# Optimization experiments

Measured on AMD Instinct MI355X. Metric: run time of the kernel, lower is better.

## Reference

```python
import jax, jax.numpy as jnp
import numpy as np
from functools import partial

B, T, I, H = 64, 1024, 256, 256


def _lstm_dir(x_tbi, w_ih, w_hh, b_ih, b_hh, reverse):
    """Coupled-gate LSTM over time. x_tbi: [T,B,I]. Returns hs [T,B,H], (hT, cT).

    Gates = x@W_ih^T + b_ih + h@W_hh^T + b_hh, split into (in, cell, out);
    forget = 1 - in (coupled input/forget gates).
    """
    Bn = x_tbi.shape[1]
    Hn = w_hh.shape[1]
    # Precompute input contribution for all timesteps in one big GEMM.
    gx = jnp.einsum('tbi,gi->tbg', x_tbi, w_ih) + (b_ih + b_hh)  # [T,B,3H]

    def step(carry, g):
        h, c = carry
        gates = g + h @ w_hh.T  # [B,3H]
        ig, cg, og = jnp.split(gates, 3, axis=1)
        ig = jax.nn.sigmoid(ig)
        fg = 1.0 - ig
        cg = jnp.tanh(cg)
        og = jax.nn.sigmoid(og)
        c = fg * c + ig * cg
        h = og * jnp.tanh(c)
        return (h, c), h

    h0 = jnp.zeros((Bn, Hn), dtype=x_tbi.dtype)
    c0 = jnp.zeros((Bn, Hn), dtype=x_tbi.dtype)
    # lax.scan(reverse=True) runs backward in time but stacks outputs in
    # original time order, matching ReverseLSTMLayer's reverse(outputs).
    (hT, cT), hs = jax.lax.scan(step, (h0, c0), gx, reverse=reverse)
    return hs, hT, cT


def setup_inputs() -> dict:
    key = jax.random.key(0)
    ks = jax.random.split(key, 9)
    s = 0.05  # small init scale for numerical sanity
    return {
        'X': jax.random.normal(ks[0], (B, T, I), dtype=jnp.float32),
        'wih_f': jax.random.normal(ks[1], (3 * H, I), dtype=jnp.float32) * s,
        'whh_f': jax.random.normal(ks[2], (3 * H, H), dtype=jnp.float32) * s,
        'bih_f': jax.random.normal(ks[3], (3 * H,), dtype=jnp.float32) * s,
        'bhh_f': jax.random.normal(ks[4], (3 * H,), dtype=jnp.float32) * s,
        'wih_b': jax.random.normal(ks[5], (3 * H, I), dtype=jnp.float32) * s,
        'whh_b': jax.random.normal(ks[6], (3 * H, H), dtype=jnp.float32) * s,
        'bih_b': jax.random.normal(ks[7], (3 * H,), dtype=jnp.float32) * s,
        'bhh_b': jax.random.normal(ks[8], (3 * H,), dtype=jnp.float32) * s,
    }


def reference(X, wih_f, whh_f, bih_f, bhh_f, wih_b, whh_b, bih_b, bhh_b):
    x_tbi = jnp.transpose(X, (1, 0, 2))  # [T,B,I]
    hs_f, hTf, cTf = _lstm_dir(x_tbi, wih_f, whh_f, bih_f, bhh_f, reverse=False)
    hs_b, hTb, cTb = _lstm_dir(x_tbi, wih_b, whh_b, bih_b, bhh_b, reverse=True)
    out = jnp.concatenate([hs_f, hs_b], axis=-1)  # [T,B,2H]
    hn = jnp.concatenate([hTf, hTb], axis=1)[None]  # [1,B,2H]
    cn = jnp.concatenate([cTf, cTb], axis=1)[None]
    return out, hn, cn
```

## Files before the change

### kernel.cpp

```cpp
#include <hip/hip_runtime.h>
#include <cstdint>
#include <cstddef>

#define TT 1024
#define NB 64
#define HD 256
#define NG 768

typedef short bhalf8 __attribute__((ext_vector_type(8)));
typedef float f32x4  __attribute__((ext_vector_type(4)));

__device__ __forceinline__ unsigned short f2bf(float f) {
  unsigned u = __float_as_uint(f);
  unsigned r = (u + 0x7FFFu + ((u >> 16) & 1u)) >> 16;
  return (unsigned short)r;
}
__device__ __forceinline__ float bf2f(unsigned short s) {
  return __uint_as_float(((unsigned)s) << 16);
}
__device__ __forceinline__ float sigm(float x) {
  return __builtin_amdgcn_rcpf(1.0f + __expf(-x));
}
__device__ __forceinline__ float tanh_fast(float x) {
  return 1.0f - 2.0f * __builtin_amdgcn_rcpf(__expf(2.0f * x) + 1.0f);
}

#define GX_SLICE ((size_t)TT * NG * 16)

__launch_bounds__(256, 2)
__global__ void gx_kernel(const float* __restrict__ X,
                          const float* __restrict__ wih_f, const float* __restrict__ bih_f,
                          const float* __restrict__ bhh_f,
                          const float* __restrict__ wih_b, const float* __restrict__ bih_b,
                          const float* __restrict__ bhh_b,
                          unsigned short* __restrict__ gx) {
  const int tid = threadIdx.x;
  const int n0  = blockIdx.x * 64;
  const int t0  = blockIdx.y * 4;

  __shared__ unsigned short Al[64][264];
  __shared__ unsigned short Bl[64][264];

  const int lane = tid & 63, w = tid >> 6, quad = lane >> 4, l15 = lane & 15;

  for (int dir = 0; dir < 2; ++dir) {
    const float* wih = dir ? wih_b : wih_f;
    const float* bih = dir ? bih_b : bih_f;
    const float* bhh = dir ? bhh_b : bhh_f;
    unsigned short* gxd = gx + (size_t)dir * 4 * GX_SLICE;

    __syncthreads();
#pragma unroll
    for (int i = 0; i < 16; ++i) {
      int f4  = tid + i * 256;
      int row = f4 >> 6;
      int kk  = (f4 & 63) * 4;
      float4 wv = *(const float4*)(wih + (size_t)(n0 + row) * HD + kk);
      Bl[row][kk + 0] = f2bf(wv.x); Bl[row][kk + 1] = f2bf(wv.y);
      Bl[row][kk + 2] = f2bf(wv.z); Bl[row][kk + 3] = f2bf(wv.w);
    }

    for (int tt = 0; tt < 4; ++tt) {
      const int t = t0 + tt;
      __syncthreads();
#pragma unroll
      for (int i = 0; i < 16; ++i) {
        int f4  = tid + i * 256;
        int row = f4 >> 6;
        int kk  = (f4 & 63) * 4;
        float4 xv = *(const float4*)(X + ((size_t)row * TT + t) * HD + kk);
        Al[row][kk + 0] = f2bf(xv.x); Al[row][kk + 1] = f2bf(xv.y);
        Al[row][kk + 2] = f2bf(xv.z); Al[row][kk + 3] = f2bf(xv.w);
      }
      __syncthreads();

      f32x4 acc[4];
#pragma unroll
      for (int jt = 0; jt < 4; ++jt) { acc[jt][0]=0.f; acc[jt][1]=0.f; acc[jt][2]=0.f; acc[jt][3]=0.f; }

#pragma unroll
      for (int kt = 0; kt < 8; ++kt) {
        bhalf8 a = *(const bhalf8*)&Al[16 * w + l15][kt * 32 + quad * 8];
#pragma unroll
        for (int jt = 0; jt < 4; ++jt) {
          bhalf8 b = *(const bhalf8*)&Bl[jt * 16 + l15][kt * 32 + quad * 8];
          acc[jt] = __builtin_amdgcn_mfma_f32_16x16x32_bf16(a, b, acc[jt], 0, 0, 0);
        }
      }

      unsigned short* gs = gxd + w * GX_SLICE + (size_t)t * NG * 16;
#pragma unroll
      for (int jt = 0; jt < 4; ++jt) {
        int g = n0 + jt * 16 + l15;
        float bias = bih[g] + bhh[g];
        ushort4 pk;
        pk.x = f2bf(acc[jt][0] + bias); pk.y = f2bf(acc[jt][1] + bias);
        pk.z = f2bf(acc[jt][2] + bias); pk.w = f2bf(acc[jt][3] + bias);
        *(ushort4*)(gs + g * 16 + quad * 4) = pk;
      }
    }
  }
}

__attribute__((amdgpu_flat_work_group_size(512, 512)))
__attribute__((amdgpu_waves_per_eu(2, 2)))
__global__ void rec_kernel(const float* __restrict__ whh_f,
                           const float* __restrict__ whh_b,
                           const unsigned short* __restrict__ gx,
                           float* __restrict__ out) {
  const int tid  = threadIdx.x;
  const int lane = tid & 63, w = tid >> 6, quad = lane >> 4, l15 = lane & 15;
  const int blk = blockIdx.x;
  const int dir = blk >> 2;
  const int b0  = (blk & 3) * 16;
  const float* whh = dir ? whh_b : whh_f;
  const unsigned short* gxd = gx + (size_t)dir * 4 * GX_SLICE + (size_t)(blk & 3) * GX_SLICE;
  float* hn = out + (size_t)TT * NB * 512;
  float* cn = hn + (size_t)NB * 512;

  __shared__ uint4 wlds[8][8][64];
  __shared__ uint4 hk[2][8][64];

  bhalf8 wreg[5][8];
#pragma unroll
  for (int p = 0; p < 6; ++p) {
    int n = (p >> 1) * 256 + 32 * w + (p & 1) * 16 + l15;
#pragma unroll
    for (int kt = 0; kt < 8; ++kt) {
      const float* wp = whh + (size_t)n * HD + kt * 32 + quad * 8;
      float4 v0 = *(const float4*)wp;
      float4 v1 = *(const float4*)(wp + 4);
      union { unsigned short us[8]; bhalf8 v; uint4 u; } pk;
      pk.us[0] = f2bf(v0.x); pk.us[1] = f2bf(v0.y); pk.us[2] = f2bf(v0.z); pk.us[3] = f2bf(v0.w);
      pk.us[4] = f2bf(v1.x); pk.us[5] = f2bf(v1.y); pk.us[6] = f2bf(v1.z); pk.us[7] = f2bf(v1.w);
      if (p < 5) wreg[p][kt] = pk.v;
      else       wlds[w][kt][lane] = pk.u;
    }
  }

  {
    uint4 z; z.x = z.y = z.z = z.w = 0;
    for (int i = tid; i < 8 * 64; i += 512) ((uint4*)hk[0])[i] = z;
  }

  float cstate[2][4];
#pragma unroll
  for (int jn = 0; jn < 2; ++jn)
#pragma unroll
    for (int r = 0; r < 4; ++r) cstate[jn][r] = 0.0f;

  int goff[6];
#pragma unroll
  for (int p = 0; p < 6; ++p) {
    int g = (p >> 1) * 256 + 32 * w + (p & 1) * 16 + l15;
    goff[p] = g * 16 + quad * 4;
  }

  __syncthreads();

  const unsigned short* gptr = gxd + (size_t)(dir ? (TT - 1) : 0) * NG * 16;
  const ptrdiff_t gstep = dir ? -(ptrdiff_t)((size_t)NG * 16) : (ptrdiff_t)((size_t)NG * 16);

  ushort4 gxv[6];
#pragma unroll
  for (int p = 0; p < 6; ++p) gxv[p] = *(const ushort4*)(gptr + goff[p]);

#pragma unroll 2
  for (int s = 0; s < TT; ++s) {
    const int tr = dir ? (TT - 1 - s) : s;
    const int pb = s & 1;

    f32x4 acc[6];
#pragma unroll
    for (int p = 0; p < 6; ++p) {
      acc[p][0] = bf2f(gxv[p].x); acc[p][1] = bf2f(gxv[p].y);
      acc[p][2] = bf2f(gxv[p].z); acc[p][3] = bf2f(gxv[p].w);
    }
    gptr += gstep;
#pragma unroll
    for (int p = 0; p < 6; ++p) gxv[p] = *(const ushort4*)(gptr + goff[p]);

#pragma unroll
    for (int kt = 0; kt < 8; ++kt) {
      bhalf8 a = __builtin_bit_cast(bhalf8, hk[pb][kt][lane]);
#pragma unroll
      for (int p = 0; p < 5; ++p)
        acc[p] = __builtin_amdgcn_mfma_f32_16x16x32_bf16(a, wreg[p][kt], acc[p], 0, 0, 0);
      acc[5] = __builtin_amdgcn_mfma_f32_16x16x32_bf16(
          a, __builtin_bit_cast(bhalf8, wlds[w][kt][lane]), acc[5], 0, 0, 0);
    }

    float* orow = out + ((size_t)tr * NB + b0 + quad * 4) * 512 + dir * 256 + 32 * w + l15;
    unsigned short* hnext = (unsigned short*)hk[pb ^ 1][w];
#pragma unroll
    for (int jn = 0; jn < 2; ++jn) {
#pragma unroll
      for (int r = 0; r < 4; ++r) {
        float ig = sigm(acc[jn][r]);
        float cg = tanh_fast(acc[2 + jn][r]);
        float og = sigm(acc[4 + jn][r]);
        float cp = cstate[jn][r];
        float cv = __builtin_fmaf(ig, cg - cp, cp);
        cstate[jn][r] = cv;
        float hv = og * tanh_fast(cv);
        orow[(size_t)r * 512 + jn * 16] = hv;
        int chunk = (jn * 2 + (l15 >> 3)) * 16 + quad * 4 + r;
        hnext[chunk * 8 + (l15 & 7)] = f2bf(hv);
        if (s == TT - 1) {
          int brow = b0 + quad * 4 + r;
          int col  = 32 * w + jn * 16 + l15;
          hn[(size_t)brow * 512 + dir * 256 + col] = hv;
          cn[(size_t)brow * 512 + dir * 256 + col] = cv;
        }
      }
    }
    __syncthreads();
  }
}

extern "C" void kernel_launch(void* const* d_in, const int* in_sizes, int n_in,
                              void* d_out, int out_size, void* d_ws, size_t ws_size,
                              hipStream_t stream) {
  const float* X     = (const float*)d_in[0];
  const float* wih_f = (const float*)d_in[1];
  const float* whh_f = (const float*)d_in[2];
  const float* bih_f = (const float*)d_in[3];
  const float* bhh_f = (const float*)d_in[4];
  const float* wih_b = (const float*)d_in[5];
  const float* whh_b = (const float*)d_in[6];
  const float* bih_b = (const float*)d_in[7];
  const float* bhh_b = (const float*)d_in[8];
  float* out = (float*)d_out;
  unsigned short* gxbuf = (unsigned short*)d_ws;

  dim3 g1(NG / 64, TT / 4);
  gx_kernel<<<g1, 256, 0, stream>>>(X, wih_f, bih_f, bhh_f, wih_b, bih_b, bhh_b, gxbuf);
  rec_kernel<<<8, 512, 0, stream>>>(whh_f, whh_b, gxbuf, out);
}
```

Before: 2.264 ms.

## Prescale gates by log2e, batch reciprocals, use packed bf16 conversions

Folds the log2(e) (and 2*log2(e) for the cell gate) scaling into the input and recurrent weights and biases, so the recurrent step can call exp2 directly on pre-scaled gate values. It replaces the per-element reciprocals with a batched four-way reciprocal trick (one rcp per four values) and uses the hardware packed bf16 conversion instead of manual rounding. It also replaces the per-step output-row address computation with an incremented pointer. These changes shorten the serial per-timestep elementwise critical path, at the cost of extra rounding from the product-of-four reciprocal and clamping exponent inputs to ±24.

```diff
diff --git a/kernel.cpp b/kernel.cpp
--- a/kernel.cpp
+++ b/kernel.cpp
@@ -10,19 +10,32 @@
 typedef short bhalf8 __attribute__((ext_vector_type(8)));
 typedef float f32x4  __attribute__((ext_vector_type(4)));
 
-__device__ __forceinline__ unsigned short f2bf(float f) {
-  unsigned u = __float_as_uint(f);
-  unsigned r = (u + 0x7FFFu + ((u >> 16) & 1u)) >> 16;
-  return (unsigned short)r;
-}
+#define LOG2E  1.4426950408889634f
+#define LOG2E2 2.8853900817779268f
+
 __device__ __forceinline__ float bf2f(unsigned short s) {
   return __uint_as_float(((unsigned)s) << 16);
 }
-__device__ __forceinline__ float sigm(float x) {
-  return __builtin_amdgcn_rcpf(1.0f + __expf(-x));
-}
-__device__ __forceinline__ float tanh_fast(float x) {
-  return 1.0f - 2.0f * __builtin_amdgcn_rcpf(__expf(2.0f * x) + 1.0f);
+__device__ __forceinline__ unsigned cvt_pk_bf16(float lo, float hi) {
+  unsigned r;
+  asm("v_cvt_pk_bf16_f32 %0, %1, %2" : "=v"(r) : "v"(lo), "v"(hi));
+  return r;
+}
+__device__ __forceinline__ float clamp24(float x) {
+  return fminf(fmaxf(x, -24.0f), 24.0f);
+}
+__device__ __forceinline__ void inv4(float d0, float d1, float d2, float d3,
+                                     float& i0, float& i1, float& i2, float& i3) {
+  float p2 = d0 * d1;
+  float p3 = p2 * d2;
+  float p4 = p3 * d3;
+  float r  = __builtin_amdgcn_rcpf(p4);
+  i3 = r * p3;
+  float r3 = r * d3;
+  i2 = r3 * p2;
+  float r2 = r3 * d2;
+  i1 = r2 * d0;
+  i0 = r2 * d1;
 }
 
 #define GX_SLICE ((size_t)TT * NG * 16)
@@ -42,6 +55,7 @@
   __shared__ unsigned short Bl[64][264];
 
   const int lane = tid & 63, w = tid >> 6, quad = lane >> 4, l15 = lane & 15;
+  const float wsc = (n0 >= 256 && n0 < 512) ? LOG2E2 : LOG2E;
 
   for (int dir = 0; dir < 2; ++dir) {
     const float* wih = dir ? wih_b : wih_f;
@@ -56,8 +70,10 @@
       int row = f4 >> 6;
       int kk  = (f4 & 63) * 4;
       float4 wv = *(const float4*)(wih + (size_t)(n0 + row) * HD + kk);
-      Bl[row][kk + 0] = f2bf(wv.x); Bl[row][kk + 1] = f2bf(wv.y);
-      Bl[row][kk + 2] = f2bf(wv.z); Bl[row][kk + 3] = f2bf(wv.w);
+      uint2 p;
+      p.x = cvt_pk_bf16(wv.x * wsc, wv.y * wsc);
+      p.y = cvt_pk_bf16(wv.z * wsc, wv.w * wsc);
+      *(uint2*)&Bl[row][kk] = p;
     }
 
     for (int tt = 0; tt < 4; ++tt) {
@@ -69,8 +85,10 @@
         int row = f4 >> 6;
         int kk  = (f4 & 63) * 4;
         float4 xv = *(const float4*)(X + ((size_t)row * TT + t) * HD + kk);
-        Al[row][kk + 0] = f2bf(xv.x); Al[row][kk + 1] = f2bf(xv.y);
-        Al[row][kk + 2] = f2bf(xv.z); Al[row][kk + 3] = f2bf(xv.w);
+        uint2 p;
+        p.x = cvt_pk_bf16(xv.x, xv.y);
+        p.y = cvt_pk_bf16(xv.z, xv.w);
+        *(uint2*)&Al[row][kk] = p;
       }
       __syncthreads();
 
@@ -92,11 +110,11 @@
 #pragma unroll
       for (int jt = 0; jt < 4; ++jt) {
         int g = n0 + jt * 16 + l15;
-        float bias = bih[g] + bhh[g];
-        ushort4 pk;
-        pk.x = f2bf(acc[jt][0] + bias); pk.y = f2bf(acc[jt][1] + bias);
-        pk.z = f2bf(acc[jt][2] + bias); pk.w = f2bf(acc[jt][3] + bias);
-        *(ushort4*)(gs + g * 16 + quad * 4) = pk;
+        float bias = (bih[g] + bhh[g]) * wsc;
+        uint2 p;
+        p.x = cvt_pk_bf16(acc[jt][0] + bias, acc[jt][1] + bias);
+        p.y = cvt_pk_bf16(acc[jt][2] + bias, acc[jt][3] + bias);
+        *(uint2*)(gs + g * 16 + quad * 4) = p;
       }
     }
   }
@@ -125,14 +143,17 @@
 #pragma unroll
   for (int p = 0; p < 6; ++p) {
     int n = (p >> 1) * 256 + 32 * w + (p & 1) * 16 + l15;
+    const float wscp = ((p >> 1) == 1) ? LOG2E2 : LOG2E;
 #pragma unroll
     for (int kt = 0; kt < 8; ++kt) {
       const float* wp = whh + (size_t)n * HD + kt * 32 + quad * 8;
       float4 v0 = *(const float4*)wp;
       float4 v1 = *(const float4*)(wp + 4);
-      union { unsigned short us[8]; bhalf8 v; uint4 u; } pk;
-      pk.us[0] = f2bf(v0.x); pk.us[1] = f2bf(v0.y); pk.us[2] = f2bf(v0.z); pk.us[3] = f2bf(v0.w);
-      pk.us[4] = f2bf(v1.x); pk.us[5] = f2bf(v1.y); pk.us[6] = f2bf(v1.z); pk.us[7] = f2bf(v1.w);
+      union { bhalf8 v; uint4 u; } pk;
+      pk.u.x = cvt_pk_bf16(v0.x * wscp, v0.y * wscp);
+      pk.u.y = cvt_pk_bf16(v0.z * wscp, v0.w * wscp);
+      pk.u.z = cvt_pk_bf16(v1.x * wscp, v1.y * wscp);
+      pk.u.w = cvt_pk_bf16(v1.z * wscp, v1.w * wscp);
       if (p < 5) wreg[p][kt] = pk.v;
       else       wlds[w][kt][lane] = pk.u;
     }
@@ -161,13 +182,16 @@
   const unsigned short* gptr = gxd + (size_t)(dir ? (TT - 1) : 0) * NG * 16;
   const ptrdiff_t gstep = dir ? -(ptrdiff_t)((size_t)NG * 16) : (ptrdiff_t)((size_t)NG * 16);
 
+  float* orow = out + ((size_t)(dir ? (TT - 1) : 0) * NB + b0 + quad * 4) * 512
+                + dir * 256 + 32 * w + l15;
+  const ptrdiff_t ostep = dir ? -(ptrdiff_t)(NB * 512) : (ptrdiff_t)(NB * 512);
+
   ushort4 gxv[6];
 #pragma unroll
   for (int p = 0; p < 6; ++p) gxv[p] = *(const ushort4*)(gptr + goff[p]);
 
 #pragma unroll 2
   for (int s = 0; s < TT; ++s) {
-    const int tr = dir ? (TT - 1 - s) : s;
     const int pb = s & 1;
 
     f32x4 acc[6];
@@ -190,30 +214,62 @@
           a, __builtin_bit_cast(bhalf8, wlds[w][kt][lane]), acc[5], 0, 0, 0);
     }
 
-    float* orow = out + ((size_t)tr * NB + b0 + quad * 4) * 512 + dir * 256 + 32 * w + l15;
     unsigned short* hnext = (unsigned short*)hk[pb ^ 1][w];
 #pragma unroll
     for (int jn = 0; jn < 2; ++jn) {
+      float ei[4], ec[4], eo[4];
 #pragma unroll
       for (int r = 0; r < 4; ++r) {
-        float ig = sigm(acc[jn][r]);
-        float cg = tanh_fast(acc[2 + jn][r]);
-        float og = sigm(acc[4 + jn][r]);
+        ei[r] = __builtin_amdgcn_exp2f(clamp24(-acc[jn][r]));
+        ec[r] = __builtin_amdgcn_exp2f(clamp24( acc[2 + jn][r]));
+        eo[r] = __builtin_amdgcn_exp2f(clamp24(-acc[4 + jn][r]));
+      }
+      float ig[4], tc[4], og[4];
+      inv4(1.f + ei[0], 1.f + ei[1], 1.f + ei[2], 1.f + ei[3],
+           ig[0], ig[1], ig[2], ig[3]);
+      inv4(1.f + ec[0], 1.f + ec[1], 1.f + ec[2], 1.f + ec[3],
+           tc[0], tc[1], tc[2], tc[3]);
+      inv4(1.f + eo[0], 1.f + eo[1], 1.f + eo[2], 1.f + eo[3],
+           og[0], og[1], og[2], og[3]);
+      float cvv[4], et[4];
+#pragma unroll
+      for (int r = 0; r < 4; ++r) {
+        float cg = __builtin_fmaf(-2.f, tc[r], 1.f);
         float cp = cstate[jn][r];
-        float cv = __builtin_fmaf(ig, cg - cp, cp);
+        float cv = __builtin_fmaf(ig[r], cg - cp, cp);
         cstate[jn][r] = cv;
-        float hv = og * tanh_fast(cv);
-        orow[(size_t)r * 512 + jn * 16] = hv;
-        int chunk = (jn * 2 + (l15 >> 3)) * 16 + quad * 4 + r;
-        hnext[chunk * 8 + (l15 & 7)] = f2bf(hv);
+        cvv[r] = cv;
+        et[r] = __builtin_amdgcn_exp2f(cv * LOG2E2);
+      }
+      float it4[4];
+      inv4(1.f + et[0], 1.f + et[1], 1.f + et[2], 1.f + et[3],
+           it4[0], it4[1], it4[2], it4[3]);
+      float hv[4];
+#pragma unroll
+      for (int r = 0; r < 4; ++r)
+        hv[r] = og[r] * __builtin_fmaf(-2.f, it4[r], 1.f);
+
+      unsigned short* hbj = hnext + (size_t)(((jn * 2 + (l15 >> 3)) * 16 + quad * 4) * 8)
+                            + (l15 & 7);
+      unsigned u01 = cvt_pk_bf16(hv[0], hv[1]);
+      unsigned u23 = cvt_pk_bf16(hv[2], hv[3]);
+      hbj[0]  = (unsigned short)u01;
+      hbj[8]  = (unsigned short)(u01 >> 16);
+      hbj[16] = (unsigned short)u23;
+      hbj[24] = (unsigned short)(u23 >> 16);
+
+#pragma unroll
+      for (int r = 0; r < 4; ++r) {
+        orow[(size_t)r * 512 + jn * 16] = hv[r];
         if (s == TT - 1) {
           int brow = b0 + quad * 4 + r;
           int col  = 32 * w + jn * 16 + l15;
-          hn[(size_t)brow * 512 + dir * 256 + col] = hv;
-          cn[(size_t)brow * 512 + dir * 256 + col] = cv;
+          hn[(size_t)brow * 512 + dir * 256 + col] = hv[r];
+          cn[(size_t)brow * 512 + dir * 256 + col] = cvv[r];
         }
       }
     }
+    orow += ostep;
     __syncthreads();
   }
 }
```

Result: slower. 2.314 ms (+2.2%).
